# Optimization experiments

Hardware: AMD Instinct MI355X
Metric: run time of the kernel (lower is better)

## Reference

```python
import jax, jax.numpy as jnp
import numpy as np

H = 8  # number of heads


def setup_inputs() -> dict:
    key = jax.random.key(0)
    ks = jax.random.split(key, 5)
    B, L, D = 4, 2048, 512
    scale = 1.0 / np.sqrt(D)
    return {
        "query": jax.random.normal(ks[0], (B, L, D), dtype=jnp.float32),
        "keys": jax.random.normal(ks[1], (B, L, D), dtype=jnp.float32),
        "Wq": jax.random.normal(ks[2], (D, D), dtype=jnp.float32) * scale,
        "Wk": jax.random.normal(ks[3], (D, D), dtype=jnp.float32) * scale,
        "Wv": jax.random.normal(ks[4], (D, D), dtype=jnp.float32) * scale,
    }


def reference(query, keys, Wq, Wk, Wv):
    B, Lq, D = query.shape
    Lk = keys.shape[1]
    dh = D // H
    # Linear layers (torch nn.Linear: y = x @ W.T), then split heads.
    Q = (query @ Wq.T).reshape(B, Lq, H, dh)
    K = (keys @ Wk.T).reshape(B, Lk, H, dh)
    V = (keys @ Wv.T).reshape(B, Lk, H, dh)
    # NOTE: original scales by sqrt(key_dim) == sqrt(D), not sqrt(head_dim).
    inv_scale = 1.0 / jnp.sqrt(jnp.float32(D))
    scores = jnp.einsum("bqhd,bkhd->bhqk", Q, K) * inv_scale  # [B,H,Lq,Lk]
    attn = jax.nn.softmax(scores, axis=-1)
    # dropout_p = 0 (eval); no dropout applied.
    out = jnp.einsum("bhqk,bkhd->bqhd", attn, V).reshape(B, Lq, D)
    return out + query  # residual
```

## Files before the change

kernel.cpp:

```cpp
#include <hip/hip_runtime.h>

typedef unsigned short u16;
typedef unsigned int   u32;
typedef short  s16x8  __attribute__((ext_vector_type(8)));
typedef float  f32x16 __attribute__((ext_vector_type(16)));

__device__ __forceinline__ u16 f2bf(float f) {
    union { u32 i; float f; } x; x.f = f;
    return (u16)((x.i + 0x8000u) >> 16);
}
__device__ __forceinline__ u32 pk_hi16(float a, float b) {
    union { float f; u32 u; } ua, ub; ua.f = a; ub.f = b;
    return __builtin_amdgcn_perm(ub.u + 0x8000u, ua.u + 0x8000u, 0x07060302u);
}

#define PD 512

__global__ __launch_bounds__(256) void proj_mfma(
    const float* __restrict__ query, const float* __restrict__ keys,
    const float* __restrict__ Wq, const float* __restrict__ Wk, const float* __restrict__ Wv,
    u16* __restrict__ Qo, u16* __restrict__ Ko, u16* __restrict__ Vt)
{
    const int z = blockIdx.z;
    const float* __restrict__ X = (z == 0) ? query : keys;
    const float* __restrict__ W = (z == 0) ? Wq : ((z == 1) ? Wk : Wv);
    const int bx = blockIdx.x;
    const int by = blockIdx.y;

    const float* __restrict__ Amat = (z < 2) ? X : W;
    const float* __restrict__ Bmat = (z < 2) ? W : X;
    const int a0 = ((z < 2) ? bx : by) * 128;
    const int b0 = ((z < 2) ? by : bx) * 128;

    __shared__ u16 As[128][40];
    __shared__ u16 Bs[128][40];

    const int tid  = threadIdx.x;
    const int wave = tid >> 6, lane = tid & 63;
    const int wm = wave >> 1, wn = wave & 1;
    const int l31 = lane & 31, lh = lane >> 5;

    const int srow = tid >> 1;
    const int sk   = (tid & 1) * 16;

    f32x16 acc[2][2];
    #pragma unroll
    for (int i = 0; i < 2; ++i)
        #pragma unroll
        for (int j = 0; j < 2; ++j)
            #pragma unroll
            for (int r = 0; r < 16; ++r) acc[i][j][r] = 0.f;

    float4 ra[4], rb[4];
    {
        const float* ap = Amat + (size_t)(a0 + srow) * PD + sk;
        const float* bp = Bmat + (size_t)(b0 + srow) * PD + sk;
        #pragma unroll
        for (int i = 0; i < 4; ++i) {
            ra[i] = *(const float4*)(ap + 4*i);
            rb[i] = *(const float4*)(bp + 4*i);
        }
    }

    for (int k0 = 0; k0 < PD; k0 += 32) {
        __syncthreads();
        {
            u32 aw[8], bw[8];
            #pragma unroll
            for (int i = 0; i < 4; ++i) {
                aw[2*i]   = pk_hi16(ra[i].x, ra[i].y);
                aw[2*i+1] = pk_hi16(ra[i].z, ra[i].w);
                bw[2*i]   = pk_hi16(rb[i].x, rb[i].y);
                bw[2*i+1] = pk_hi16(rb[i].z, rb[i].w);
            }
            *(uint4*)&As[srow][sk]     = *(uint4*)&aw[0];
            *(uint4*)&As[srow][sk + 8] = *(uint4*)&aw[4];
            *(uint4*)&Bs[srow][sk]     = *(uint4*)&bw[0];
            *(uint4*)&Bs[srow][sk + 8] = *(uint4*)&bw[4];
        }
        if (k0 + 32 < PD) {
            const float* ap = Amat + (size_t)(a0 + srow) * PD + (k0 + 32) + sk;
            const float* bp = Bmat + (size_t)(b0 + srow) * PD + (k0 + 32) + sk;
            #pragma unroll
            for (int i = 0; i < 4; ++i) {
                ra[i] = *(const float4*)(ap + 4*i);
                rb[i] = *(const float4*)(bp + 4*i);
            }
        }
        __syncthreads();

        #pragma unroll
        for (int ks = 0; ks < 2; ++ks) {
            s16x8 af[2], bfr[2];
            #pragma unroll
            for (int mf = 0; mf < 2; ++mf) {
                uint4 v = *(uint4*)&As[wm*64 + mf*32 + l31][ks*16 + lh*8];
                af[mf] = *(s16x8*)&v;
            }
            #pragma unroll
            for (int nf = 0; nf < 2; ++nf) {
                uint4 v = *(uint4*)&Bs[wn*64 + nf*32 + l31][ks*16 + lh*8];
                bfr[nf] = *(s16x8*)&v;
            }
            #pragma unroll
            for (int mf = 0; mf < 2; ++mf)
                #pragma unroll
                for (int nf = 0; nf < 2; ++nf)
                    acc[mf][nf] = __builtin_amdgcn_mfma_f32_32x32x16_bf16(
                        af[mf], bfr[nf], acc[mf][nf], 0, 0, 0);
        }
    }

    const float osc = (z == 0) ? (0.044194173824159216f * 1.4426950408889634f) : 1.0f;
    u16* __restrict__ O = (z == 0) ? Qo : Ko;
    #pragma unroll
    for (int mf = 0; mf < 2; ++mf)
        #pragma unroll
        for (int nf = 0; nf < 2; ++nf)
            #pragma unroll
            for (int r = 0; r < 16; ++r) {
                const int mi = a0 + wm*64 + mf*32 + (r & 3) + 8*(r >> 2) + 4*lh;
                const int ni = b0 + wn*64 + nf*32 + l31;
                const u16 v = f2bf(acc[mf][nf][r] * osc);
                if (z < 2) {
                    O[(size_t)mi * PD + ni] = v;
                } else {
                    const int bb_ = ni >> 11, ll = ni & 2047;
                    Vt[((size_t)(bb_ * 512 + mi)) * 2048 + ll] = v;
                }
            }
}

__global__ __launch_bounds__(256) void attn_mfma(
    const u16* __restrict__ Qp, const u16* __restrict__ Kp, const u16* __restrict__ Vt,
    const float* __restrict__ query, float* __restrict__ out)
{
    const int qt = blockIdx.x;
    const int h  = blockIdx.y;
    const int b  = blockIdx.z;
    const int q0 = qt * 128;
    const int L = 2048;

    __shared__ uint4 lds_u4[36864 / 16];
    u16* Ks   = (u16*)lds_u4;
    u16* Vts  = Ks + 64 * 72;
    u16* P2a  = Vts + 64 * 72;
    float* Oe = (float*)lds_u4;

    const int tid  = threadIdx.x;
    const int wave = tid >> 6, lane = tid & 63;
    const int l31 = lane & 31, lh = lane >> 5;
    u16* P2 = P2a + wave * 32 * 72;

    const int qrow = b * L + q0 + wave * 32 + l31;
    s16x8 qf[4];
    #pragma unroll
    for (int ds = 0; ds < 4; ++ds) {
        uint4 v = *(const uint4*)(Qp + (size_t)qrow * PD + h*64 + ds*16 + lh*8);
        qf[ds] = *(s16x8*)&v;
    }

    f32x16 ot[2];
    #pragma unroll
    for (int mf = 0; mf < 2; ++mf)
        #pragma unroll
        for (int r = 0; r < 16; ++r) ot[mf][r] = 0.f;
    float m_i = -INFINITY, l_i = 0.f;

    const int srow = tid >> 2;
    const int sc   = (tid & 3) * 16;

    uint4 rk0, rk1, rv0, rv1;
    {
        const u16* kp = Kp + (size_t)(b*L + srow) * PD + h*64 + sc;
        const u16* vp = Vt + ((size_t)((b*8 + h)*64 + srow)) * 2048 + sc;
        rk0 = *(const uint4*)kp;      rk1 = *(const uint4*)(kp + 8);
        rv0 = *(const uint4*)vp;      rv1 = *(const uint4*)(vp + 8);
    }

    for (int k0 = 0; k0 < L; k0 += 64) {
        __syncthreads();
        *(uint4*)&Ks [srow*72 + sc]     = rk0;
        *(uint4*)&Ks [srow*72 + sc + 8] = rk1;
        *(uint4*)&Vts[srow*72 + sc]     = rv0;
        *(uint4*)&Vts[srow*72 + sc + 8] = rv1;
        if (k0 + 64 < L) {
            const u16* kp = Kp + (size_t)(b*L + (k0+64) + srow) * PD + h*64 + sc;
            const u16* vp = Vt + ((size_t)((b*8 + h)*64 + srow)) * 2048 + (k0+64) + sc;
            rk0 = *(const uint4*)kp;  rk1 = *(const uint4*)(kp + 8);
            rv0 = *(const uint4*)vp;  rv1 = *(const uint4*)(vp + 8);
        }
        __syncthreads();

        f32x16 s[2];
        #pragma unroll
        for (int kf = 0; kf < 2; ++kf) {
            #pragma unroll
            for (int r = 0; r < 16; ++r) s[kf][r] = 0.f;
            #pragma unroll
            for (int ds = 0; ds < 4; ++ds) {
                uint4 av = *(uint4*)&Ks[(kf*32 + l31)*72 + ds*16 + lh*8];
                s[kf] = __builtin_amdgcn_mfma_f32_32x32x16_bf16(
                    *(s16x8*)&av, qf[ds], s[kf], 0, 0, 0);
            }
        }

        float rm = -INFINITY;
        #pragma unroll
        for (int kf = 0; kf < 2; ++kf)
            #pragma unroll
            for (int r = 0; r < 16; ++r) rm = fmaxf(rm, s[kf][r]);
        rm = fmaxf(rm, __shfl_xor(rm, 32));
        const float m_new = fmaxf(m_i, rm);
        const float alpha = __builtin_amdgcn_exp2f(m_i - m_new);
        float rs = 0.f;
        #pragma unroll
        for (int kf = 0; kf < 2; ++kf)
            #pragma unroll
            for (int g = 0; g < 4; ++g) {
                float p0 = __builtin_amdgcn_exp2f(s[kf][4*g+0] - m_new);
                float p1 = __builtin_amdgcn_exp2f(s[kf][4*g+1] - m_new);
                float p2 = __builtin_amdgcn_exp2f(s[kf][4*g+2] - m_new);
                float p3 = __builtin_amdgcn_exp2f(s[kf][4*g+3] - m_new);
                rs += (p0 + p1) + (p2 + p3);
                uint2 w2;
                w2.x = pk_hi16(p0, p1);
                w2.y = pk_hi16(p2, p3);
                *(uint2*)&P2[l31*72 + kf*32 + g*8 + lh*4] = w2;
            }
        rs += __shfl_xor(rs, 32);
        l_i = l_i * alpha + rs;
        m_i = m_new;
        #pragma unroll
        for (int mf = 0; mf < 2; ++mf)
            #pragma unroll
            for (int r = 0; r < 16; ++r) ot[mf][r] *= alpha;

        #pragma unroll
        for (int ks = 0; ks < 4; ++ks) {
            uint4 bv = *(uint4*)&P2[l31*72 + ks*16 + lh*8];
            s16x8 bfr = *(s16x8*)&bv;
            #pragma unroll
            for (int mf = 0; mf < 2; ++mf) {
                uint4 av = *(uint4*)&Vts[(mf*32 + l31)*72 + ks*16 + lh*8];
                ot[mf] = __builtin_amdgcn_mfma_f32_32x32x16_bf16(
                    *(s16x8*)&av, bfr, ot[mf], 0, 0, 0);
            }
        }
    }

    __syncthreads();
    const float inv_l = 1.0f / l_i;
    #pragma unroll
    for (int mf = 0; mf < 2; ++mf)
        #pragma unroll
        for (int g = 0; g < 4; ++g) {
            float4 v;
            v.x = ot[mf][g*4+0] * inv_l;
            v.y = ot[mf][g*4+1] * inv_l;
            v.z = ot[mf][g*4+2] * inv_l;
            v.w = ot[mf][g*4+3] * inv_l;
            const int dh0 = mf*32 + 8*g + 4*lh;
            *(float4*)&Oe[(wave*32 + l31)*68 + dh0] = v;
        }
    __syncthreads();
    {
        const int r  = tid >> 1;
        const int c0 = (tid & 1) * 32;
        const size_t gb = ((size_t)(b*L + q0 + r)) * PD + h*64 + c0;
        #pragma unroll
        for (int i = 0; i < 8; ++i) {
            float4 ov = *(float4*)&Oe[r*68 + c0 + 4*i];
            float4 qv = *(const float4*)(query + gb + 4*i);
            ov.x += qv.x; ov.y += qv.y; ov.z += qv.z; ov.w += qv.w;
            *(float4*)(out + gb + 4*i) = ov;
        }
    }
}

extern "C" void kernel_launch(void* const* d_in, const int* in_sizes, int n_in,
                              void* d_out, int out_size, void* d_ws, size_t ws_size,
                              hipStream_t stream) {
    const float* query = (const float*)d_in[0];
    const float* keys  = (const float*)d_in[1];
    const float* Wq    = (const float*)d_in[2];
    const float* Wk    = (const float*)d_in[3];
    const float* Wv    = (const float*)d_in[4];
    float* out = (float*)d_out;

    u16* Qp = (u16*)d_ws;
    u16* Kp = Qp + (size_t)8192 * 512;
    u16* Vt = Kp + (size_t)8192 * 512;

    proj_mfma<<<dim3(64, 4, 3), 256, 0, stream>>>(query, keys, Wq, Wk, Wv, Qp, Kp, Vt);
    attn_mfma<<<dim3(16, 8, 4), 256, 0, stream>>>(Qp, Kp, Vt, query, out);
}
```

Baseline: 177.9 us.

## Feed softmax probabilities to PV MFMA directly from registers via 32x32x8 bf16

The PV product now uses the K=8 bf16 MFMA, whose B-operand layout matches the S accumulator layout. Packed probabilities can therefore be fed straight from registers instead of round-tripping through a per-wave LDS buffer. This removes the LDS write and read of P in every tile. In exchange it issues twice as many MFMAs at half the K depth, which may have lower throughput on CDNA4 than the K=16 instruction, and V is read from LDS in smaller 8-byte loads.

```diff
diff --git a/kernel.cpp b/kernel.cpp
--- a/kernel.cpp
+++ b/kernel.cpp
@@ -2,6 +2,7 @@
 
 typedef unsigned short u16;
 typedef unsigned int   u32;
+typedef short  s16x4  __attribute__((ext_vector_type(4)));
 typedef short  s16x8  __attribute__((ext_vector_type(8)));
 typedef float  f32x16 __attribute__((ext_vector_type(16)));
 
@@ -13,6 +14,16 @@
     union { float f; u32 u; } ua, ub; ua.f = a; ub.f = b;
     return __builtin_amdgcn_perm(ub.u + 0x8000u, ua.u + 0x8000u, 0x07060302u);
 }
+
+#if __has_builtin(__builtin_amdgcn_mfma_f32_32x32x8bf16_1k)
+#define HAVE_X8 1
+#define MFMA8(a, b, c) __builtin_amdgcn_mfma_f32_32x32x8bf16_1k((a), (b), (c), 0, 0, 0)
+#elif __has_builtin(__builtin_amdgcn_mfma_f32_32x32x8_bf16)
+#define HAVE_X8 1
+#define MFMA8(a, b, c) __builtin_amdgcn_mfma_f32_32x32x8_bf16((a), (b), (c), 0, 0, 0)
+#else
+#define HAVE_X8 0
+#endif
 
 #define PD 512
 
@@ -144,13 +155,17 @@
     __shared__ uint4 lds_u4[36864 / 16];
     u16* Ks   = (u16*)lds_u4;
     u16* Vts  = Ks + 64 * 72;
+#if !HAVE_X8
     u16* P2a  = Vts + 64 * 72;
+#endif
     float* Oe = (float*)lds_u4;
 
     const int tid  = threadIdx.x;
     const int wave = tid >> 6, lane = tid & 63;
     const int l31 = lane & 31, lh = lane >> 5;
+#if !HAVE_X8
     u16* P2 = P2a + wave * 32 * 72;
+#endif
 
     const int qrow = b * L + q0 + wave * 32 + l31;
     s16x8 qf[4];
@@ -214,6 +229,7 @@
         const float m_new = fmaxf(m_i, rm);
         const float alpha = __builtin_amdgcn_exp2f(m_i - m_new);
         float rs = 0.f;
+        u32 pq[2][4][2];
         #pragma unroll
         for (int kf = 0; kf < 2; ++kf)
             #pragma unroll
@@ -223,10 +239,12 @@
                 float p2 = __builtin_amdgcn_exp2f(s[kf][4*g+2] - m_new);
                 float p3 = __builtin_amdgcn_exp2f(s[kf][4*g+3] - m_new);
                 rs += (p0 + p1) + (p2 + p3);
-                uint2 w2;
-                w2.x = pk_hi16(p0, p1);
-                w2.y = pk_hi16(p2, p3);
+                pq[kf][g][0] = pk_hi16(p0, p1);
+                pq[kf][g][1] = pk_hi16(p2, p3);
+#if !HAVE_X8
+                uint2 w2; w2.x = pq[kf][g][0]; w2.y = pq[kf][g][1];
                 *(uint2*)&P2[l31*72 + kf*32 + g*8 + lh*4] = w2;
+#endif
             }
         rs += __shfl_xor(rs, 32);
         l_i = l_i * alpha + rs;
@@ -236,6 +254,22 @@
             #pragma unroll
             for (int r = 0; r < 16; ++r) ot[mf][r] *= alpha;
 
+#if HAVE_X8
+        #pragma unroll
+        for (int kf = 0; kf < 2; ++kf)
+            #pragma unroll
+            for (int g = 0; g < 4; ++g) {
+                union { u32 w[2]; s16x4 v; } bu;
+                bu.w[0] = pq[kf][g][0];
+                bu.w[1] = pq[kf][g][1];
+                #pragma unroll
+                for (int mf = 0; mf < 2; ++mf) {
+                    union { uint2 u; s16x4 v; } au;
+                    au.u = *(uint2*)&Vts[(mf*32 + l31)*72 + kf*32 + g*8 + lh*4];
+                    ot[mf] = MFMA8(au.v, bu.v, ot[mf]);
+                }
+            }
+#else
         #pragma unroll
         for (int ks = 0; ks < 4; ++ks) {
             uint4 bv = *(uint4*)&P2[l31*72 + ks*16 + lh*8];
@@ -247,6 +281,7 @@
                     *(s16x8*)&av, bfr, ot[mf], 0, 0, 0);
             }
         }
+#endif
     }
 
     __syncthreads();
```

New measurement: 178.5 us. Within noise of the previous version (+0.3%).
